# Performance work log

Measured on AMD Instinct MI355X. Metric: run time of the kernel, lower is better.

The kernel has to match this reference:

```python
import jax, jax.numpy as jnp
import numpy as np


def setup_inputs() -> dict:
    key = jax.random.key(0)
    kq, kk, kv = jax.random.split(key, 3)
    N, L, S, H, D = 4, 2048, 2048, 8, 64
    queries = jax.random.normal(kq, (N, L, H, D), dtype=jnp.float32)
    keys = jax.random.normal(kk, (N, S, H, D), dtype=jnp.float32)
    values = jax.random.normal(kv, (N, S, H, D), dtype=jnp.float32)
    return {"queries": queries, "keys": keys, "values": values}


def reference(queries, keys, values):
    # QK^T: [N, L, S, H]
    qk = jnp.einsum('nlhd,nshd->nlsh', queries, keys)
    softmax_temp = 1.0 / np.sqrt(queries.shape[3]).astype(np.float32)
    attn = jax.nn.softmax(softmax_temp * qk, axis=2)  # softmax over S
    # dropout with drop_rate=0.0 is identity
    out = jnp.einsum('nlsh,nshd->nlhd', attn, values)
    return out
```

## Files before the change

### kernel.cpp

```cpp
#include <hip/hip_runtime.h>
#include <hip/hip_bf16.h>
#include <stdint.h>


typedef __bf16 bf16x8 __attribute__((ext_vector_type(8)));
typedef float  f32x16 __attribute__((ext_vector_type(16)));

#define N_ 4
#define L_ 2048
#define S_ 2048
#define H_ 8
#define D_ 64
#define NH 32
#define QBLK 128
#define KVBLK 64
#define NKV 32
#define TILE_BF16 8192
#define PLANE_BF16 (NKV * TILE_BF16)
#define SCALE_LOG2E 0.18033688011112042f

static __device__ __forceinline__ uint32_t pkbf(float lo, float hi) {
    uint16_t l = __builtin_bit_cast(uint16_t, (__bf16)lo);
    uint16_t h = __builtin_bit_cast(uint16_t, (__bf16)hi);
    return (uint32_t)l | ((uint32_t)h << 16);
}

__global__ __launch_bounds__(256) void prep_k(const float* __restrict__ K,
                                              __bf16* __restrict__ F) {
    const int ch   = blockIdx.x * 256 + threadIdx.x;
    const int nh   = ch >> 14;
    const int kv   = (ch >> 9) & 31;
    const int r    = ch & 511;
    const int sl   = r >> 3;
    const int slot = r & 7;
    const int n = nh >> 3, h = nh & 7;
    const float* p = K + ((size_t)(n * 2048 + kv * 64 + sl) * 8 + h) * 64 + slot * 8;
    float4 a = *(const float4*)p;
    float4 b = *(const float4*)(p + 4);
    bf16x8 v;
    v[0] = (__bf16)a.x; v[1] = (__bf16)a.y; v[2] = (__bf16)a.z; v[3] = (__bf16)a.w;
    v[4] = (__bf16)b.x; v[5] = (__bf16)b.y; v[6] = (__bf16)b.z; v[7] = (__bf16)b.w;
    const int st = sl >> 5, c = sl & 31, ks = slot >> 1, hh = slot & 1;
    *(bf16x8*)(F + (size_t)nh * PLANE_BF16 + kv * TILE_BF16
                 + (st * 4 + ks) * 512 + (hh * 32 + c) * 8) = v;
}

__global__ __launch_bounds__(256) void prep_v(const float* __restrict__ V,
                                              __bf16* __restrict__ F) {
    __shared__ __align__(16) __bf16 T[64 * 64];
    const int tid = threadIdx.x;
    const int bid = blockIdx.x;
    const int nh  = bid >> 5;
    const int kv  = bid & 31;
    const int n   = nh >> 3, h = nh & 7;
    const int s0  = kv * 64;
#pragma unroll
    for (int it = 0; it < 16; ++it) {
        const int idx = it * 256 + tid;
        const int sl  = idx >> 6;
        const int d   = idx & 63;
        float v = V[(size_t)(n * 2048 + s0 + sl) * 512 + h * 64 + d];
        T[d * 64 + (((sl >> 3) ^ (d & 7)) * 8) + (sl & 7)] = (__bf16)v;
    }
    __syncthreads();
#pragma unroll
    for (int it = 0; it < 2; ++it) {
        const int idx = it * 256 + tid;
        const int d   = idx >> 3;
        const int sc  = idx & 7;
        bf16x8 v = *(const bf16x8*)&T[d * 64 + ((sc ^ (d & 7)) * 8)];
        const int dt = d >> 5, c = d & 31, kt = sc >> 1, hh = sc & 1;
        *(bf16x8*)(F + (size_t)nh * PLANE_BF16 + kv * TILE_BF16
                     + (8 + dt * 4 + kt) * 512 + (hh * 32 + c) * 8) = v;
    }
}

__global__ __launch_bounds__(256, 2) void fattn(const float* __restrict__ Q,
                                                const __bf16* __restrict__ F,
                                                float* __restrict__ Out) {
    const int tid  = threadIdx.x;
    const int wave = tid >> 6;
    const int lane = tid & 63;
    const int hh   = lane >> 5;
    const int c    = lane & 31;

    int bid = blockIdx.x;
    bid = (bid & 7) * 64 + (bid >> 3);
    const int nh = bid >> 4;
    const int qt = bid & 15;
    const int n  = nh >> 3, hd = nh & 7;
    const int q0 = qt * QBLK;

    const float*  Qp = Q   + (size_t)n * 1048576 + hd * 64;
    float*        Op = Out + (size_t)n * 1048576 + hd * 64;
    const __bf16* Pl = F + (size_t)nh * PLANE_BF16;

    bf16x8 qf[4];
    {
        const float* qp = Qp + (size_t)(q0 + wave * 32 + c) * 512;
#pragma unroll
        for (int ks = 0; ks < 4; ++ks) {
            float4 a = *(const float4*)(qp + ks * 16 + hh * 8);
            float4 b = *(const float4*)(qp + ks * 16 + hh * 8 + 4);
            bf16x8 v;
            v[0] = (__bf16)(a.x * SCALE_LOG2E); v[1] = (__bf16)(a.y * SCALE_LOG2E);
            v[2] = (__bf16)(a.z * SCALE_LOG2E); v[3] = (__bf16)(a.w * SCALE_LOG2E);
            v[4] = (__bf16)(b.x * SCALE_LOG2E); v[5] = (__bf16)(b.y * SCALE_LOG2E);
            v[6] = (__bf16)(b.z * SCALE_LOG2E); v[7] = (__bf16)(b.w * SCALE_LOG2E);
            qf[ks] = v;
        }
    }

    float m_r = -1e30f, lsum = 0.f;
    f32x16 oacc[2];
#pragma unroll
    for (int dt = 0; dt < 2; ++dt)
#pragma unroll
        for (int r = 0; r < 16; ++r) oacc[dt][r] = 0.f;

    bf16x8 kA[8], kB[8], vv[8];

    auto LK = [&](bf16x8 (&dst)[8], int kv) {
        const bf16x8* t = (const bf16x8*)(Pl + (size_t)kv * TILE_BF16);
#pragma unroll
        for (int f = 0; f < 8; ++f) dst[f] = t[f * 64 + lane];
    };
    auto LV = [&](bf16x8 (&dst)[8], int kv) {
        const bf16x8* t = (const bf16x8*)(Pl + (size_t)kv * TILE_BF16) + 512;
#pragma unroll
        for (int f = 0; f < 8; ++f) dst[f] = t[f * 64 + lane];
    };

    auto ITER = [&](bf16x8 (&kf)[8], bf16x8 (&vf)[8]) {
        f32x16 sacc[2];
#pragma unroll
        for (int st = 0; st < 2; ++st)
#pragma unroll
            for (int r = 0; r < 16; ++r) sacc[st][r] = 0.f;
        __builtin_amdgcn_s_setprio(1);
#pragma unroll
        for (int ks = 0; ks < 4; ++ks)
#pragma unroll
            for (int st = 0; st < 2; ++st)
                sacc[st] = __builtin_amdgcn_mfma_f32_32x32x16_bf16(kf[st * 4 + ks], qf[ks], sacc[st], 0, 0, 0);
        __builtin_amdgcn_s_setprio(0);

        float mx[16];
#pragma unroll
        for (int i = 0; i < 16; ++i) mx[i] = fmaxf(sacc[0][i], sacc[1][i]);
#pragma unroll
        for (int w = 8; w >= 1; w >>= 1)
#pragma unroll
            for (int i = 0; i < w; ++i) mx[i] = fmaxf(mx[i], mx[i + w]);
        float tm = fmaxf(mx[0], __shfl_xor(mx[0], 32, 64));
        if (!__all(tm <= m_r + 8.0f)) {
            const float mnew = fmaxf(m_r, tm);
            const float al   = __builtin_amdgcn_exp2f(m_r - mnew);
            m_r = mnew;
            lsum *= al;
#pragma unroll
            for (int dt = 0; dt < 2; ++dt)
#pragma unroll
                for (int r = 0; r < 16; ++r) oacc[dt][r] *= al;
        }
#pragma unroll
        for (int st = 0; st < 2; ++st)
#pragma unroll
            for (int r = 0; r < 16; ++r)
                sacc[st][r] = __builtin_amdgcn_exp2f(sacc[st][r] - m_r);
        float sm[16];
#pragma unroll
        for (int i = 0; i < 16; ++i) sm[i] = sacc[0][i] + sacc[1][i];
#pragma unroll
        for (int w = 8; w >= 1; w >>= 1)
#pragma unroll
            for (int i = 0; i < w; ++i) sm[i] += sm[i + w];
        lsum += sm[0];

        bf16x8 pf[4];
#pragma unroll
        for (int st = 0; st < 2; ++st) {
            uint32_t W[8];
#pragma unroll
            for (int i = 0; i < 8; ++i) W[i] = pkbf(sacc[st][2 * i], sacc[st][2 * i + 1]);
#pragma unroll
            for (int kk = 0; kk < 2; ++kk) {
                uint32_t a0 = W[4 * kk + 0], b0 = W[4 * kk + 2];
                uint32_t a1 = W[4 * kk + 1], b1 = W[4 * kk + 3];
                asm volatile("v_permlane32_swap_b32 %0, %1" : "+v"(a0), "+v"(b0));
                asm volatile("v_permlane32_swap_b32 %0, %1" : "+v"(a1), "+v"(b1));
                union { uint32_t u[4]; bf16x8 v; } pu;
                pu.u[0] = a0; pu.u[1] = a1; pu.u[2] = b0; pu.u[3] = b1;
                pf[st * 2 + kk] = pu.v;
            }
        }

        __builtin_amdgcn_s_setprio(1);
#pragma unroll
        for (int kt = 0; kt < 4; ++kt)
#pragma unroll
            for (int dt = 0; dt < 2; ++dt)
                oacc[dt] = __builtin_amdgcn_mfma_f32_32x32x16_bf16(vf[dt * 4 + kt], pf[kt], oacc[dt], 0, 0, 0);
        __builtin_amdgcn_s_setprio(0);
    };

    LK(kA, 0);
    for (int kv = 0; kv < NKV; kv += 2) {
        LV(vv, kv);
        LK(kB, kv + 1);
        ITER(kA, vv);
        LV(vv, kv + 1);
        LK(kA, kv + 2 < NKV ? kv + 2 : NKV - 1);
        ITER(kB, vv);
    }

    lsum += __shfl_xor(lsum, 32, 64);
    const float inv = 1.0f / lsum;
    float* op = Op + (size_t)(q0 + wave * 32 + c) * 512;
#pragma unroll
    for (int dt = 0; dt < 2; ++dt) {
#pragma unroll
        for (int rr = 0; rr < 4; ++rr) {
            float4 o = { oacc[dt][4 * rr + 0] * inv, oacc[dt][4 * rr + 1] * inv,
                         oacc[dt][4 * rr + 2] * inv, oacc[dt][4 * rr + 3] * inv };
            *(float4*)(op + dt * 32 + rr * 8 + hh * 4) = o;
        }
    }
}

extern "C" void kernel_launch(void* const* d_in, const int* in_sizes, int n_in,
                              void* d_out, int out_size, void* d_ws, size_t ws_size,
                              hipStream_t stream) {
    const float* Q = (const float*)d_in[0];
    const float* K = (const float*)d_in[1];
    const float* V = (const float*)d_in[2];
    float* Out = (float*)d_out;
    __bf16* F = (__bf16*)d_ws;

    prep_k<<<dim3(2048), dim3(256), 0, stream>>>(K, F);
    prep_v<<<dim3(1024), dim3(256), 0, stream>>>(V, F);
    fattn <<<dim3(512),  dim3(256), 0, stream>>>(Q, F, Out);
}
```

Measured before the change: 70.95 us.

## Split KV sequence into two independent online-softmax streams per wave

The KV plane is re-laid out as 32-key tiles, and each wave now processes two independent streams: keys 0-1023 and keys 1024-2047. Each stream keeps its own running max, sum and output accumulators, and the two are merged at the end. This makes two independent MFMA/softmax dependency chains interleave, hiding latency, and software-prefetches the next tile's K and V into registers. It costs more accumulator registers (four output tiles), which may pressure occupancy at two blocks per CU, plus a final merge.

```diff
diff --git a/kernel.cpp b/kernel.cpp
--- a/kernel.cpp
+++ b/kernel.cpp
@@ -13,10 +13,9 @@
 #define D_ 64
 #define NH 32
 #define QBLK 128
-#define KVBLK 64
-#define NKV 32
-#define TILE_BF16 8192
-#define PLANE_BF16 (NKV * TILE_BF16)
+#define NT32 64
+#define TILE32 4096
+#define PLANE_BF16 (NT32 * TILE32)
 #define SCALE_LOG2E 0.18033688011112042f
 
 static __device__ __forceinline__ uint32_t pkbf(float lo, float hi) {
@@ -25,24 +24,63 @@
     return (uint32_t)l | ((uint32_t)h << 16);
 }
 
+static __device__ __forceinline__ float tmax16(const f32x16& s) {
+    float a[8];
+#pragma unroll
+    for (int i = 0; i < 8; ++i) a[i] = fmaxf(s[i], s[i + 8]);
+#pragma unroll
+    for (int w = 4; w >= 1; w >>= 1)
+#pragma unroll
+        for (int i = 0; i < w; ++i) a[i] = fmaxf(a[i], a[i + w]);
+    return a[0];
+}
+
+static __device__ __forceinline__ float tsum16(const f32x16& s) {
+    float a[8];
+#pragma unroll
+    for (int i = 0; i < 8; ++i) a[i] = s[i] + s[i + 8];
+#pragma unroll
+    for (int w = 4; w >= 1; w >>= 1)
+#pragma unroll
+        for (int i = 0; i < w; ++i) a[i] += a[i + w];
+    return a[0];
+}
+
+static __device__ __forceinline__ void packP(const f32x16& s, bf16x8 (&pf)[2]) {
+    uint32_t W[8];
+#pragma unroll
+    for (int i = 0; i < 8; ++i) W[i] = pkbf(s[2 * i], s[2 * i + 1]);
+#pragma unroll
+    for (int kt = 0; kt < 2; ++kt) {
+        uint32_t a0 = W[4 * kt + 0], b0 = W[4 * kt + 2];
+        uint32_t a1 = W[4 * kt + 1], b1 = W[4 * kt + 3];
+        asm volatile("v_permlane32_swap_b32 %0, %1" : "+v"(a0), "+v"(b0));
+        asm volatile("v_permlane32_swap_b32 %0, %1" : "+v"(a1), "+v"(b1));
+        union { uint32_t u[4]; bf16x8 v; } pu;
+        pu.u[0] = a0; pu.u[1] = a1; pu.u[2] = b0; pu.u[3] = b1;
+        pf[kt] = pu.v;
+    }
+}
+
 __global__ __launch_bounds__(256) void prep_k(const float* __restrict__ K,
                                               __bf16* __restrict__ F) {
     const int ch   = blockIdx.x * 256 + threadIdx.x;
     const int nh   = ch >> 14;
-    const int kv   = (ch >> 9) & 31;
-    const int r    = ch & 511;
-    const int sl   = r >> 3;
-    const int slot = r & 7;
+    const int r    = ch & 16383;
+    const int t    = r >> 8;
+    const int rr   = r & 255;
+    const int sl   = rr >> 3;
+    const int slot = rr & 7;
     const int n = nh >> 3, h = nh & 7;
-    const float* p = K + ((size_t)(n * 2048 + kv * 64 + sl) * 8 + h) * 64 + slot * 8;
+    const float* p = K + ((size_t)(n * 2048 + t * 32 + sl) * 8 + h) * 64 + slot * 8;
     float4 a = *(const float4*)p;
     float4 b = *(const float4*)(p + 4);
     bf16x8 v;
     v[0] = (__bf16)a.x; v[1] = (__bf16)a.y; v[2] = (__bf16)a.z; v[3] = (__bf16)a.w;
     v[4] = (__bf16)b.x; v[5] = (__bf16)b.y; v[6] = (__bf16)b.z; v[7] = (__bf16)b.w;
-    const int st = sl >> 5, c = sl & 31, ks = slot >> 1, hh = slot & 1;
-    *(bf16x8*)(F + (size_t)nh * PLANE_BF16 + kv * TILE_BF16
-                 + (st * 4 + ks) * 512 + (hh * 32 + c) * 8) = v;
+    const int ks = slot >> 1, hh = slot & 1;
+    *(bf16x8*)(F + (size_t)nh * PLANE_BF16 + t * TILE32
+                 + ks * 512 + (hh * 32 + sl) * 8) = v;
 }
 
 __global__ __launch_bounds__(256) void prep_v(const float* __restrict__ V,
@@ -51,9 +89,9 @@
     const int tid = threadIdx.x;
     const int bid = blockIdx.x;
     const int nh  = bid >> 5;
-    const int kv  = bid & 31;
+    const int t0  = (bid & 31) * 2;
     const int n   = nh >> 3, h = nh & 7;
-    const int s0  = kv * 64;
+    const int s0  = (bid & 31) * 64;
 #pragma unroll
     for (int it = 0; it < 16; ++it) {
         const int idx = it * 256 + tid;
@@ -69,9 +107,10 @@
         const int d   = idx >> 3;
         const int sc  = idx & 7;
         bf16x8 v = *(const bf16x8*)&T[d * 64 + ((sc ^ (d & 7)) * 8)];
-        const int dt = d >> 5, c = d & 31, kt = sc >> 1, hh = sc & 1;
-        *(bf16x8*)(F + (size_t)nh * PLANE_BF16 + kv * TILE_BF16
-                     + (8 + dt * 4 + kt) * 512 + (hh * 32 + c) * 8) = v;
+        const int dt = d >> 5, c = d & 31;
+        const int tile = t0 + (sc >> 2), kt = (sc >> 1) & 1, hh = sc & 1;
+        *(bf16x8*)(F + (size_t)nh * PLANE_BF16 + tile * TILE32
+                     + (4 + dt * 2 + kt) * 512 + (hh * 32 + c) * 8) = v;
     }
 }
 
@@ -93,7 +132,7 @@
 
     const float*  Qp = Q   + (size_t)n * 1048576 + hd * 64;
     float*        Op = Out + (size_t)n * 1048576 + hd * 64;
-    const __bf16* Pl = F + (size_t)nh * PLANE_BF16;
+    const bf16x8* Tb = (const bf16x8*)(F + (size_t)nh * PLANE_BF16);
 
     bf16x8 qf[4];
     {
@@ -111,120 +150,104 @@
         }
     }
 
-    float m_r = -1e30f, lsum = 0.f;
-    f32x16 oacc[2];
-#pragma unroll
-    for (int dt = 0; dt < 2; ++dt)
-#pragma unroll
-        for (int r = 0; r < 16; ++r) oacc[dt][r] = 0.f;
-
-    bf16x8 kA[8], kB[8], vv[8];
-
-    auto LK = [&](bf16x8 (&dst)[8], int kv) {
-        const bf16x8* t = (const bf16x8*)(Pl + (size_t)kv * TILE_BF16);
-#pragma unroll
-        for (int f = 0; f < 8; ++f) dst[f] = t[f * 64 + lane];
-    };
-    auto LV = [&](bf16x8 (&dst)[8], int kv) {
-        const bf16x8* t = (const bf16x8*)(Pl + (size_t)kv * TILE_BF16) + 512;
-#pragma unroll
-        for (int f = 0; f < 8; ++f) dst[f] = t[f * 64 + lane];
-    };
-
-    auto ITER = [&](bf16x8 (&kf)[8], bf16x8 (&vf)[8]) {
-        f32x16 sacc[2];
-#pragma unroll
-        for (int st = 0; st < 2; ++st)
-#pragma unroll
-            for (int r = 0; r < 16; ++r) sacc[st][r] = 0.f;
+    float mA = -1e30f, lA = 0.f, mB = -1e30f, lB = 0.f;
+    f32x16 oA0, oA1, oB0, oB1;
+#pragma unroll
+    for (int r = 0; r < 16; ++r) { oA0[r] = 0.f; oA1[r] = 0.f; oB0[r] = 0.f; oB1[r] = 0.f; }
+
+    bf16x8 kA[4], vA[4], kB[4], vB[4];
+#pragma unroll
+    for (int f = 0; f < 4; ++f) {
+        kA[f] = Tb[0 * 512 + f * 64 + lane];
+        vA[f] = Tb[0 * 512 + 256 + f * 64 + lane];
+        kB[f] = Tb[32 * 512 + f * 64 + lane];
+        vB[f] = Tb[32 * 512 + 256 + f * 64 + lane];
+    }
+
+    for (int t = 0; t < 32; ++t) {
+        const int tn = (t + 1 < 32) ? t + 1 : 31;
+
+        f32x16 sA, sB;
+#pragma unroll
+        for (int r = 0; r < 16; ++r) { sA[r] = 0.f; sB[r] = 0.f; }
         __builtin_amdgcn_s_setprio(1);
 #pragma unroll
-        for (int ks = 0; ks < 4; ++ks)
-#pragma unroll
-            for (int st = 0; st < 2; ++st)
-                sacc[st] = __builtin_amdgcn_mfma_f32_32x32x16_bf16(kf[st * 4 + ks], qf[ks], sacc[st], 0, 0, 0);
+        for (int ks = 0; ks < 4; ++ks) {
+            sA = __builtin_amdgcn_mfma_f32_32x32x16_bf16(kA[ks], qf[ks], sA, 0, 0, 0);
+            sB = __builtin_amdgcn_mfma_f32_32x32x16_bf16(kB[ks], qf[ks], sB, 0, 0, 0);
+        }
         __builtin_amdgcn_s_setprio(0);
 
-        float mx[16];
-#pragma unroll
-        for (int i = 0; i < 16; ++i) mx[i] = fmaxf(sacc[0][i], sacc[1][i]);
-#pragma unroll
-        for (int w = 8; w >= 1; w >>= 1)
-#pragma unroll
-            for (int i = 0; i < w; ++i) mx[i] = fmaxf(mx[i], mx[i + w]);
-        float tm = fmaxf(mx[0], __shfl_xor(mx[0], 32, 64));
-        if (!__all(tm <= m_r + 8.0f)) {
-            const float mnew = fmaxf(m_r, tm);
-            const float al   = __builtin_amdgcn_exp2f(m_r - mnew);
-            m_r = mnew;
-            lsum *= al;
-#pragma unroll
-            for (int dt = 0; dt < 2; ++dt)
-#pragma unroll
-                for (int r = 0; r < 16; ++r) oacc[dt][r] *= al;
-        }
-#pragma unroll
-        for (int st = 0; st < 2; ++st)
-#pragma unroll
-            for (int r = 0; r < 16; ++r)
-                sacc[st][r] = __builtin_amdgcn_exp2f(sacc[st][r] - m_r);
-        float sm[16];
-#pragma unroll
-        for (int i = 0; i < 16; ++i) sm[i] = sacc[0][i] + sacc[1][i];
-#pragma unroll
-        for (int w = 8; w >= 1; w >>= 1)
-#pragma unroll
-            for (int i = 0; i < w; ++i) sm[i] += sm[i + w];
-        lsum += sm[0];
-
-        bf16x8 pf[4];
-#pragma unroll
-        for (int st = 0; st < 2; ++st) {
-            uint32_t W[8];
-#pragma unroll
-            for (int i = 0; i < 8; ++i) W[i] = pkbf(sacc[st][2 * i], sacc[st][2 * i + 1]);
-#pragma unroll
-            for (int kk = 0; kk < 2; ++kk) {
-                uint32_t a0 = W[4 * kk + 0], b0 = W[4 * kk + 2];
-                uint32_t a1 = W[4 * kk + 1], b1 = W[4 * kk + 3];
-                asm volatile("v_permlane32_swap_b32 %0, %1" : "+v"(a0), "+v"(b0));
-                asm volatile("v_permlane32_swap_b32 %0, %1" : "+v"(a1), "+v"(b1));
-                union { uint32_t u[4]; bf16x8 v; } pu;
-                pu.u[0] = a0; pu.u[1] = a1; pu.u[2] = b0; pu.u[3] = b1;
-                pf[st * 2 + kk] = pu.v;
+#pragma unroll
+        for (int f = 0; f < 4; ++f) {
+            kA[f] = Tb[tn * 512 + f * 64 + lane];
+            kB[f] = Tb[(tn + 32) * 512 + f * 64 + lane];
+        }
+
+        float tmA = tmax16(sA), tmB = tmax16(sB);
+        tmA = fmaxf(tmA, __shfl_xor(tmA, 32, 64));
+        tmB = fmaxf(tmB, __shfl_xor(tmB, 32, 64));
+        if (!__all((tmA <= mA + 8.0f) && (tmB <= mB + 8.0f))) {
+            const float nmA = fmaxf(mA, tmA), nmB = fmaxf(mB, tmB);
+            const float aA = __builtin_amdgcn_exp2f(mA - nmA);
+            const float aB = __builtin_amdgcn_exp2f(mB - nmB);
+            mA = nmA; mB = nmB; lA *= aA; lB *= aB;
+#pragma unroll
+            for (int r = 0; r < 16; ++r) {
+                oA0[r] *= aA; oA1[r] *= aA; oB0[r] *= aB; oB1[r] *= aB;
             }
         }
+#pragma unroll
+        for (int r = 0; r < 16; ++r) {
+            sA[r] = __builtin_amdgcn_exp2f(sA[r] - mA);
+            sB[r] = __builtin_amdgcn_exp2f(sB[r] - mB);
+        }
+        lA += tsum16(sA);
+        lB += tsum16(sB);
+
+        bf16x8 pfA[2], pfB[2];
+        packP(sA, pfA);
+        packP(sB, pfB);
 
         __builtin_amdgcn_s_setprio(1);
-#pragma unroll
-        for (int kt = 0; kt < 4; ++kt)
-#pragma unroll
-            for (int dt = 0; dt < 2; ++dt)
-                oacc[dt] = __builtin_amdgcn_mfma_f32_32x32x16_bf16(vf[dt * 4 + kt], pf[kt], oacc[dt], 0, 0, 0);
+        oA0 = __builtin_amdgcn_mfma_f32_32x32x16_bf16(vA[0], pfA[0], oA0, 0, 0, 0);
+        oB0 = __builtin_amdgcn_mfma_f32_32x32x16_bf16(vB[0], pfB[0], oB0, 0, 0, 0);
+        oA0 = __builtin_amdgcn_mfma_f32_32x32x16_bf16(vA[1], pfA[1], oA0, 0, 0, 0);
+        oB0 = __builtin_amdgcn_mfma_f32_32x32x16_bf16(vB[1], pfB[1], oB0, 0, 0, 0);
+        oA1 = __builtin_amdgcn_mfma_f32_32x32x16_bf16(vA[2], pfA[0], oA1, 0, 0, 0);
+        oB1 = __builtin_amdgcn_mfma_f32_32x32x16_bf16(vB[2], pfB[0], oB1, 0, 0, 0);
+        oA1 = __builtin_amdgcn_mfma_f32_32x32x16_bf16(vA[3], pfA[1], oA1, 0, 0, 0);
+        oB1 = __builtin_amdgcn_mfma_f32_32x32x16_bf16(vB[3], pfB[1], oB1, 0, 0, 0);
         __builtin_amdgcn_s_setprio(0);
-    };
-
-    LK(kA, 0);
-    for (int kv = 0; kv < NKV; kv += 2) {
-        LV(vv, kv);
-        LK(kB, kv + 1);
-        ITER(kA, vv);
-        LV(vv, kv + 1);
-        LK(kA, kv + 2 < NKV ? kv + 2 : NKV - 1);
-        ITER(kB, vv);
-    }
-
-    lsum += __shfl_xor(lsum, 32, 64);
-    const float inv = 1.0f / lsum;
+
+#pragma unroll
+        for (int f = 0; f < 4; ++f) {
+            vA[f] = Tb[tn * 512 + 256 + f * 64 + lane];
+            vB[f] = Tb[(tn + 32) * 512 + 256 + f * 64 + lane];
+        }
+    }
+
+    lA += __shfl_xor(lA, 32, 64);
+    lB += __shfl_xor(lB, 32, 64);
+    const float m  = fmaxf(mA, mB);
+    const float eA = __builtin_amdgcn_exp2f(mA - m);
+    const float eB = __builtin_amdgcn_exp2f(mB - m);
+    const float inv = 1.0f / (lA * eA + lB * eB);
+    const float cA = eA * inv, cB = eB * inv;
+
     float* op = Op + (size_t)(q0 + wave * 32 + c) * 512;
 #pragma unroll
-    for (int dt = 0; dt < 2; ++dt) {
-#pragma unroll
-        for (int rr = 0; rr < 4; ++rr) {
-            float4 o = { oacc[dt][4 * rr + 0] * inv, oacc[dt][4 * rr + 1] * inv,
-                         oacc[dt][4 * rr + 2] * inv, oacc[dt][4 * rr + 3] * inv };
-            *(float4*)(op + dt * 32 + rr * 8 + hh * 4) = o;
-        }
+    for (int rr = 0; rr < 4; ++rr) {
+        float4 o0 = { oA0[4 * rr + 0] * cA + oB0[4 * rr + 0] * cB,
+                      oA0[4 * rr + 1] * cA + oB0[4 * rr + 1] * cB,
+                      oA0[4 * rr + 2] * cA + oB0[4 * rr + 2] * cB,
+                      oA0[4 * rr + 3] * cA + oB0[4 * rr + 3] * cB };
+        *(float4*)(op + rr * 8 + hh * 4) = o0;
+        float4 o1 = { oA1[4 * rr + 0] * cA + oB1[4 * rr + 0] * cB,
+                      oA1[4 * rr + 1] * cA + oB1[4 * rr + 1] * cB,
+                      oA1[4 * rr + 2] * cA + oB1[4 * rr + 2] * cB,
+                      oA1[4 * rr + 3] * cA + oB1[4 * rr + 3] * cB };
+        *(float4*)(op + 32 + rr * 8 + hh * 4) = o1;
     }
 }
 
```

Result: slower. 73.66 us (+3.8%).
